# Performance work log

Measured on AMD Instinct MI355X. Metric: run time of the kernel, lower is better.

## Reference

```python
import jax, jax.numpy as jnp
import numpy as np

T = 8192        # tokens (batch*seq)
D = 1024        # d_model
H = 4096        # expert hidden = 4*d_model
E = 16          # num_expert
K = 2           # moe_top_k


def setup_inputs() -> dict:
    key = jax.random.key(0)
    ks = jax.random.split(key, 7)
    s_in = 1.0 / np.sqrt(D)
    s_h = 1.0 / np.sqrt(H)
    return {
        "moe_inp": jax.random.normal(ks[0], (T, D), dtype=jnp.float32),
        "Wg": jax.random.normal(ks[1], (D, E), dtype=jnp.float32) * s_in,
        "bg": jnp.zeros((E,), dtype=jnp.float32),
        "W1": jax.random.normal(ks[2], (E, D, H), dtype=jnp.float32) * s_in,
        "b1": jnp.zeros((E, H), dtype=jnp.float32),
        "W2": jax.random.normal(ks[3], (E, H, D), dtype=jnp.float32) * s_h,
        "b2": jnp.zeros((E, D), dtype=jnp.float32),
    }


def reference(moe_inp, Wg, bg, W1, b1, W2, b2):
    # --- NaiveGate: linear -> top-k -> softmax over selected logits ---
    logits = moe_inp @ Wg + bg                      # [T, E]
    topk_val, topk_idx = jax.lax.top_k(logits, K)   # [T, K]
    gate_score = jax.nn.softmax(topk_val, axis=-1)  # [T, K]

    # Per-(token, expert) combine weight: sum of gate scores of slots routed to e.
    # Equivalent to scatter(dispatch) -> expert MLP -> gather(combine) weighted sum.
    onehot = jax.nn.one_hot(topk_idx, E, dtype=moe_inp.dtype)  # [T, K, E]
    comb_w = jnp.einsum('tk,tke->te', gate_score, onehot)      # [T, E]

    out = jnp.zeros_like(moe_inp)
    for e in range(E):  # fixed small expert count
        h = jax.nn.relu(moe_inp @ W1[e] + b1[e])   # [T, H]
        y = h @ W2[e] + b2[e]                      # [T, D]
        out = out + comb_w[:, e:e + 1] * y
    return out
```

## Files before the change

kernel.cpp:

```cpp
#include <hip/hip_runtime.h>
#include <hip/hip_bf16.h>
#include <stdint.h>


#define Tn 8192
#define Dn 1024
#define Hn 4096
#define En 16

typedef __attribute__((ext_vector_type(8))) short bf16x8;
typedef __attribute__((ext_vector_type(4))) float f32x4;

__device__ __forceinline__ unsigned short f2bf(float f) {
    union { __hip_bfloat16 h; unsigned short u; } cv;
    cv.h = __float2bfloat16(f);
    return cv.u;
}
__device__ __forceinline__ float bf2f(unsigned short u) {
    union { unsigned int i; float f; } cv;
    cv.i = ((unsigned int)u) << 16;
    return cv.f;
}

__device__ __forceinline__ void gload_lds16(const void* gptr, void* lptr) {
    __builtin_amdgcn_global_load_lds(
        (const __attribute__((address_space(1))) uint32_t*)gptr,
        (__attribute__((address_space(3))) uint32_t*)lptr, 16, 0, 0);
}

__device__ __forceinline__ int find_e(const int* __restrict__ mb, int gm) {
    int e = 0;
#pragma unroll
    for (int i = 1; i < En; i++) e += (mb[i] <= gm) ? 1 : 0;
    return e;
}

__device__ __forceinline__ void waitvm0()  { asm volatile("s_waitcnt vmcnt(0)" ::: "memory"); }
__device__ __forceinline__ void barrier_raw() { asm volatile("s_barrier" ::: "memory"); }

__device__ __forceinline__ bool better(float va, int ia, float vb, int ib) {
    return (va > vb) || (va == vb && ia < ib);
}

__global__ __launch_bounds__(256) void gate_kernel(
    const float* __restrict__ x, const float* __restrict__ Wg,
    const float* __restrict__ bg,
    int* cnt, int* tok_e, int* tok_pos, float* tok_w)
{
    __shared__ float wgt[16 * 1028];
    int tid = threadIdx.x;
    int t0 = blockIdx.x * 16;

#pragma unroll
    for (int i = 0; i < 64; i++) {
        int idx = i * 256 + tid;
        int k = idx >> 4, e = idx & 15;
        wgt[e * 1028 + k] = Wg[idx];
    }
    __syncthreads();

    int tok = tid >> 4, e = tid & 15;
    const float4* xr = reinterpret_cast<const float4*>(x + (size_t)(t0 + tok) * Dn);
    const float4* wr = reinterpret_cast<const float4*>(&wgt[e * 1028]);
    float acc = 0.f;
#pragma unroll 8
    for (int q = 0; q < 256; q++) {
        float4 xv = xr[q], wv = wr[q];
        acc += xv.x * wv.x + xv.y * wv.y + xv.z * wv.z + xv.w * wv.w;
    }
    acc += bg[e];

    float v0 = acc, v1 = -1e30f;
    int i0 = e, i1 = -1;
#pragma unroll
    for (int m = 1; m < 16; m <<= 1) {
        float ov0 = __shfl_xor(v0, m, 16); int oi0 = __shfl_xor(i0, m, 16);
        float ov1 = __shfl_xor(v1, m, 16); int oi1 = __shfl_xor(i1, m, 16);
        if (better(ov0, oi0, v0, i0)) {
            if (better(v0, i0, ov1, oi1)) { v1 = v0; i1 = i0; }
            else                          { v1 = ov1; i1 = oi1; }
            v0 = ov0; i0 = oi0;
        } else if (better(ov0, oi0, v1, i1)) {
            v1 = ov0; i1 = oi0;
        }
    }
    if (e == 0) {
        float ex = __expf(v1 - v0);
        float w0 = 1.f / (1.f + ex);
        float w1 = ex / (1.f + ex);
        int p0 = atomicAdd(&cnt[i0], 1);
        int p1 = atomicAdd(&cnt[i1], 1);
        int t = t0 + tok;
        tok_e[t * 2 + 0] = i0; tok_e[t * 2 + 1] = i1;
        tok_pos[t * 2 + 0] = p0; tok_pos[t * 2 + 1] = p1;
        tok_w[t * 2 + 0] = w0; tok_w[t * 2 + 1] = w1;
    }
}

__global__ void scan_kernel(const int* cnt, int* base, int* mb)
{
    if (threadIdx.x == 0 && blockIdx.x == 0) {
        int b = 0, m = 0;
        for (int e = 0; e < En; e++) {
            base[e] = b; mb[e] = m;
            b += cnt[e];
            m += (cnt[e] + 255) >> 8;
        }
        base[En] = b; mb[En] = m;
    }
}

__global__ __launch_bounds__(256) void gather_kernel(
    const float* __restrict__ x, const int* tok_e, const int* tok_pos,
    const int* base, unsigned short* xg)
{
    int t = blockIdx.x; int tid = threadIdx.x;
    int e0 = tok_e[2 * t], e1 = tok_e[2 * t + 1];
    int r0 = base[e0] + tok_pos[2 * t];
    int r1 = base[e1] + tok_pos[2 * t + 1];
    float4 v = *reinterpret_cast<const float4*>(x + (size_t)t * Dn + tid * 4);
    ushort4 u;
    u.x = f2bf(v.x); u.y = f2bf(v.y); u.z = f2bf(v.z); u.w = f2bf(v.w);
    *reinterpret_cast<ushort4*>(xg + (size_t)r0 * Dn + tid * 4) = u;
    *reinterpret_cast<ushort4*>(xg + (size_t)r1 * Dn + tid * 4) = u;
}

__global__ __launch_bounds__(512) void convT_kernel(
    const float* __restrict__ src, unsigned short* __restrict__ dst, int R, int C)
{
    int e = blockIdx.z;
    const float* s = src + (size_t)e * R * C;
    unsigned short* d = dst + (size_t)e * R * C;
    __shared__ float tile[64][65];
    int r0 = blockIdx.y * 64, c0 = blockIdx.x * 64;
    int tr = threadIdx.x >> 4;
    int tc4 = (threadIdx.x & 15) * 4;
    float4 v0 = *reinterpret_cast<const float4*>(s + (size_t)(r0 + tr) * C + c0 + tc4);
    float4 v1 = *reinterpret_cast<const float4*>(s + (size_t)(r0 + tr + 32) * C + c0 + tc4);
    tile[tr][tc4 + 0] = v0.x; tile[tr][tc4 + 1] = v0.y;
    tile[tr][tc4 + 2] = v0.z; tile[tr][tc4 + 3] = v0.w;
    tile[tr + 32][tc4 + 0] = v1.x; tile[tr + 32][tc4 + 1] = v1.y;
    tile[tr + 32][tc4 + 2] = v1.z; tile[tr + 32][tc4 + 3] = v1.w;
    __syncthreads();
    ushort4 u0, u1;
    u0.x = f2bf(tile[tc4 + 0][tr]);      u1.x = f2bf(tile[tc4 + 0][tr + 32]);
    u0.y = f2bf(tile[tc4 + 1][tr]);      u1.y = f2bf(tile[tc4 + 1][tr + 32]);
    u0.z = f2bf(tile[tc4 + 2][tr]);      u1.z = f2bf(tile[tc4 + 2][tr + 32]);
    u0.w = f2bf(tile[tc4 + 3][tr]);      u1.w = f2bf(tile[tc4 + 3][tr + 32]);
    *reinterpret_cast<ushort4*>(d + (size_t)(c0 + tr) * R + r0 + tc4) = u0;
    *reinterpret_cast<ushort4*>(d + (size_t)(c0 + tr + 32) * R + r0 + tc4) = u1;
}

template<bool G1>
__global__ __launch_bounds__(512, 2) void gemmk_kernel(
    const unsigned short* __restrict__ Ag, const unsigned short* __restrict__ Bg,
    const float* __restrict__ bias, unsigned short* __restrict__ outb,
    size_t ystride,
    const int* __restrict__ cnt, const int* __restrict__ base,
    const int* __restrict__ mb)
{
    constexpr int KDIM = G1 ? Dn : Hn;
    constexpr int KLEN = G1 ? Dn : (Hn / 2);
    constexpr int NOUT = G1 ? Hn : Dn;
    constexpr int NT = KLEN / 64;
    __shared__ unsigned short ldsA[2][256 * 64];
    __shared__ unsigned short ldsB[2][256 * 64];

    int bid = blockIdx.x;
    int xcd = bid & 7;
    int slot = bid >> 3;
    int totalgm = mb[En];
    int rounds = G1 ? ((totalgm + 15) >> 4) : ((totalgm + 31) >> 5);

    int tid = threadIdx.x;
    int lane = tid & 63;
    int wid = tid >> 6;
    int wr = wid >> 2, wc = wid & 3;
    int lr16 = lane & 15, lk = lane >> 4;
    int lj = lk * 4;

    int r0t = tid >> 3;
    int col8 = (tid & 7) ^ (r0t & 7);

    int aoff[8][2], boff[4][2];
#pragma unroll
    for (int m = 0; m < 8; m++) {
        int row = wr * 128 + m * 16 + lr16;
#pragma unroll
        for (int kk = 0; kk < 2; kk++)
            aoff[m][kk] = row * 64 + (((kk * 4 + lk) ^ (row & 7)) << 3);
    }
#pragma unroll
    for (int n = 0; n < 4; n++) {
        int row = wc * 64 + n * 16 + lr16;
#pragma unroll
        for (int kk = 0; kk < 2; kk++)
            boff[n][kk] = row * 64 + (((kk * 4 + lk) ^ (row & 7)) << 3);
    }

    for (int r = 0; r < rounds; r++) {
        int gm, ntile, kh;
        if constexpr (G1) {
            gm = r * 16 + (slot >> 1);
            ntile = xcd * 2 + (slot & 1);
            kh = 0;
        } else {
            gm = r * 32 + slot;
            ntile = xcd >> 1;
            kh = xcd & 1;
        }
        if (gm >= totalgm) continue;

        int e = find_e(mb, gm);
        int mtile = gm - mb[e];
        int M_e = cnt[e];
        int m0 = mtile * 256, n0 = ntile * 256;
        int kbase = kh * KLEN;
        int rowbase0 = base[e] + m0;
        const unsigned short* Ab = Ag + (size_t)rowbase0 * KDIM + kbase;
        const unsigned short* Bb = Bg + (size_t)e * NOUT * KDIM + (size_t)n0 * KDIM + kbase;

        const unsigned short* aSrc = Ab + (size_t)r0t * KDIM + col8 * 8;
        const unsigned short* bSrc = Bb + (size_t)r0t * KDIM + col8 * 8;

        f32x4 acc[8][4];
#pragma unroll
        for (int m = 0; m < 8; m++)
#pragma unroll
            for (int n = 0; n < 4; n++) acc[m][n] = (f32x4){0.f, 0.f, 0.f, 0.f};

        auto stage = [&](int t) {
            char* sa = (char*)ldsA[t & 1];
            char* sb = (char*)ldsB[t & 1];
            int k0 = t * 64;
#pragma unroll
            for (int i = 0; i < 4; i++) {
                gload_lds16(aSrc + (size_t)(i * 64) * KDIM + k0, sa + (tid + i * 512) * 16);
                gload_lds16(bSrc + (size_t)(i * 64) * KDIM + k0, sb + (tid + i * 512) * 16);
            }
        };

        stage(0);

        for (int t = 0; t < NT; ++t) {
            waitvm0();
            barrier_raw();
            if (t + 1 < NT) stage(t + 1);
            asm volatile("" ::: "memory");
            const unsigned short* sa = ldsA[t & 1];
            const unsigned short* sb = ldsB[t & 1];
#pragma unroll
            for (int kk = 0; kk < 2; kk++) {
                bf16x8 a[4], b[4];
#pragma unroll
                for (int n = 0; n < 4; n++) b[n] = *(const bf16x8*)(sb + boff[n][kk]);
#pragma unroll
                for (int m = 0; m < 4; m++) a[m] = *(const bf16x8*)(sa + aoff[m][kk]);
                __builtin_amdgcn_s_setprio(1);
#pragma unroll
                for (int m = 0; m < 4; m++)
#pragma unroll
                    for (int n = 0; n < 4; n++)
                        acc[m][n] = __builtin_amdgcn_mfma_f32_16x16x32_bf16(b[n], a[m], acc[m][n], 0, 0, 0);
                __builtin_amdgcn_s_setprio(0);
#pragma unroll
                for (int m = 0; m < 4; m++) a[m] = *(const bf16x8*)(sa + aoff[m + 4][kk]);
                __builtin_amdgcn_s_setprio(1);
#pragma unroll
                for (int m = 0; m < 4; m++)
#pragma unroll
                    for (int n = 0; n < 4; n++)
                        acc[m + 4][n] = __builtin_amdgcn_mfma_f32_16x16x32_bf16(b[n], a[m], acc[m + 4][n], 0, 0, 0);
                __builtin_amdgcn_s_setprio(0);
            }
        }

        bool addb = G1 || (kh == 0);
        const float* be = bias + (size_t)e * NOUT;
        unsigned short* ob = outb + (G1 ? 0 : (size_t)kh * ystride);
#pragma unroll
        for (int m = 0; m < 8; m++) {
            int rt = wr * 128 + m * 16 + lr16;
            if (m0 + rt < M_e) {
                size_t rowoff = (size_t)(rowbase0 + rt) * NOUT;
#pragma unroll
                for (int n = 0; n < 4; n++) {
                    int col0 = n0 + wc * 64 + n * 16 + lj;
                    float4 bs = addb ? *reinterpret_cast<const float4*>(be + col0)
                                     : (float4){0.f, 0.f, 0.f, 0.f};
                    float v0 = acc[m][n][0] + bs.x;
                    float v1 = acc[m][n][1] + bs.y;
                    float v2 = acc[m][n][2] + bs.z;
                    float v3 = acc[m][n][3] + bs.w;
                    ushort4 u;
                    if constexpr (G1) {
                        u.x = f2bf(fmaxf(v0, 0.f));
                        u.y = f2bf(fmaxf(v1, 0.f));
                        u.z = f2bf(fmaxf(v2, 0.f));
                        u.w = f2bf(fmaxf(v3, 0.f));
                    } else {
                        u.x = f2bf(v0); u.y = f2bf(v1);
                        u.z = f2bf(v2); u.w = f2bf(v3);
                    }
                    *reinterpret_cast<ushort4*>(ob + rowoff + col0) = u;
                }
            }
        }
    }
}

__global__ __launch_bounds__(256) void combine_kernel(
    const unsigned short* __restrict__ y, size_t ystride,
    const int* __restrict__ tok_e, const int* __restrict__ tok_pos,
    const int* __restrict__ base, const float* __restrict__ tok_w,
    float* __restrict__ out)
{
    int t = blockIdx.x, tid = threadIdx.x;
    int e0 = tok_e[2 * t], e1 = tok_e[2 * t + 1];
    int r0 = base[e0] + tok_pos[2 * t];
    int r1 = base[e1] + tok_pos[2 * t + 1];
    float w0 = tok_w[2 * t], w1 = tok_w[2 * t + 1];
    const unsigned short* y1 = y + ystride;
    ushort4 a0 = *reinterpret_cast<const ushort4*>(y  + (size_t)r0 * Dn + tid * 4);
    ushort4 a1 = *reinterpret_cast<const ushort4*>(y1 + (size_t)r0 * Dn + tid * 4);
    ushort4 b0 = *reinterpret_cast<const ushort4*>(y  + (size_t)r1 * Dn + tid * 4);
    ushort4 b1 = *reinterpret_cast<const ushort4*>(y1 + (size_t)r1 * Dn + tid * 4);
    float4 o;
    o.x = w0 * (bf2f(a0.x) + bf2f(a1.x)) + w1 * (bf2f(b0.x) + bf2f(b1.x));
    o.y = w0 * (bf2f(a0.y) + bf2f(a1.y)) + w1 * (bf2f(b0.y) + bf2f(b1.y));
    o.z = w0 * (bf2f(a0.z) + bf2f(a1.z)) + w1 * (bf2f(b0.z) + bf2f(b1.z));
    o.w = w0 * (bf2f(a0.w) + bf2f(a1.w)) + w1 * (bf2f(b0.w) + bf2f(b1.w));
    *reinterpret_cast<float4*>(out + (size_t)t * Dn + tid * 4) = o;
}

extern "C" void kernel_launch(void* const* d_in, const int* in_sizes, int n_in,
                              void* d_out, int out_size, void* d_ws, size_t ws_size,
                              hipStream_t stream)
{
    const float* x  = (const float*)d_in[0];
    const float* Wg = (const float*)d_in[1];
    const float* bg = (const float*)d_in[2];
    const float* W1 = (const float*)d_in[3];
    const float* b1 = (const float*)d_in[4];
    const float* W2 = (const float*)d_in[5];
    const float* b2 = (const float*)d_in[6];
    float* out = (float*)d_out;

    char* ws = (char*)d_ws;
    size_t off = 0;
    auto alloc = [&](size_t bytes) {
        size_t o = off; off += (bytes + 255) & ~(size_t)255; return o;
    };
    const int ROWS = Tn * 2;
    const int RCAP = ROWS + 256;
    const size_t YSTR = (size_t)RCAP * Dn;

    unsigned short* Wt = (unsigned short*)(ws + alloc((size_t)En * Hn * Dn * 2));
    unsigned short* xg = (unsigned short*)(ws + alloc((size_t)RCAP * Dn * 2));
    unsigned short* hg = (unsigned short*)(ws + alloc((size_t)RCAP * Hn * 2));
    unsigned short* yv = (unsigned short*)(ws + alloc(2 * YSTR * 2));
    int*   cnt     = (int*)(ws + alloc(En * 4));
    int*   base    = (int*)(ws + alloc((En + 1) * 4));
    int*   mb      = (int*)(ws + alloc((En + 1) * 4));
    int*   tok_e   = (int*)(ws + alloc(Tn * 2 * 4));
    int*   tok_pos = (int*)(ws + alloc(Tn * 2 * 4));
    float* tok_w   = (float*)(ws + alloc(Tn * 2 * 4));
    (void)ws_size; (void)in_sizes; (void)n_in; (void)out_size;

    hipMemsetAsync(cnt, 0, En * 4, stream);

    gate_kernel<<<Tn / 16, 256, 0, stream>>>(x, Wg, bg, cnt, tok_e, tok_pos, tok_w);
    scan_kernel<<<1, 64, 0, stream>>>(cnt, base, mb);
    gather_kernel<<<Tn, 256, 0, stream>>>(x, tok_e, tok_pos, base, xg);

    convT_kernel<<<dim3(Hn / 64, Dn / 64, En), 512, 0, stream>>>(W1, Wt, Dn, Hn);
    gemmk_kernel<true><<<256, 512, 0, stream>>>(
        xg, Wt, b1, hg, 0, cnt, base, mb);

    convT_kernel<<<dim3(Dn / 64, Hn / 64, En), 512, 0, stream>>>(W2, Wt, Hn, Dn);
    gemmk_kernel<false><<<256, 512, 0, stream>>>(
        hg, Wt, b2, yv, YSTR, cnt, base, mb);

    combine_kernel<<<Tn, 256, 0, stream>>>(yv, YSTR, tok_e, tok_pos, base, tok_w, out);
}
```

Baseline: 753.1 us.

## Replace 256x256 grouped GEMM with persistent 128x128 triple-buffered kernel

Replaces the 256x256-tile, 512-thread grouped expert GEMM with a 128x128-tile, 256-thread persistent kernel. It uses a 3-stage LDS pipeline with BK=32, an XCD-aware tile swizzle, and a grid-stride loop over (m,n) tiles. It also drops the split-K in the second GEMM, so combine reads a single y buffer, and expert row padding shrinks to 128. The aim is less padding waste, better load balance and higher occupancy. The trade-off is lower per-tile data reuse and more tiles to schedule.

Result: no change. 742.7 us (-1.4%).

```diff
diff --git a/kernel.cpp b/kernel.cpp
--- a/kernel.cpp
+++ b/kernel.cpp
@@ -28,6 +28,13 @@
         (__attribute__((address_space(3))) uint32_t*)lptr, 16, 0, 0);
 }
 
+__device__ __forceinline__ int swz_tile(int v, int total) {
+    int q = total >> 3, r = total & 7;
+    int x = v & 7, k = v >> 3;
+    int b = (x < r) ? x * (q + 1) : r * (q + 1) + (x - r) * q;
+    return b + k;
+}
+
 __device__ __forceinline__ int find_e(const int* __restrict__ mb, int gm) {
     int e = 0;
 #pragma unroll
@@ -35,6 +42,7 @@
     return e;
 }
 
+__device__ __forceinline__ void waitvm4()  { asm volatile("s_waitcnt vmcnt(4)" ::: "memory"); }
 __device__ __forceinline__ void waitvm0()  { asm volatile("s_waitcnt vmcnt(0)" ::: "memory"); }
 __device__ __forceinline__ void barrier_raw() { asm volatile("s_barrier" ::: "memory"); }
 
@@ -104,7 +112,7 @@
         for (int e = 0; e < En; e++) {
             base[e] = b; mb[e] = m;
             b += cnt[e];
-            m += (cnt[e] + 255) >> 8;
+            m += (cnt[e] + 127) >> 7;
         }
         base[En] = b; mb[En] = m;
     }
@@ -152,142 +160,116 @@
 }
 
 template<bool G1>
-__global__ __launch_bounds__(512, 2) void gemmk_kernel(
+__global__ __launch_bounds__(256, 3) void gemm128_kernel(
     const unsigned short* __restrict__ Ag, const unsigned short* __restrict__ Bg,
     const float* __restrict__ bias, unsigned short* __restrict__ outb,
-    size_t ystride,
     const int* __restrict__ cnt, const int* __restrict__ base,
     const int* __restrict__ mb)
 {
     constexpr int KDIM = G1 ? Dn : Hn;
-    constexpr int KLEN = G1 ? Dn : (Hn / 2);
     constexpr int NOUT = G1 ? Hn : Dn;
-    constexpr int NT = KLEN / 64;
-    __shared__ unsigned short ldsA[2][256 * 64];
-    __shared__ unsigned short ldsB[2][256 * 64];
-
-    int bid = blockIdx.x;
-    int xcd = bid & 7;
-    int slot = bid >> 3;
+    constexpr int NTN = NOUT / 128;
+    constexpr int NT = KDIM / 32;
+    __shared__ unsigned short ldsA[3][128 * 32];
+    __shared__ unsigned short ldsB[3][128 * 32];
+
     int totalgm = mb[En];
-    int rounds = G1 ? ((totalgm + 15) >> 4) : ((totalgm + 31) >> 5);
+    int total = totalgm * NTN;
 
     int tid = threadIdx.x;
     int lane = tid & 63;
-    int wid = tid >> 6;
-    int wr = wid >> 2, wc = wid & 3;
+    int w = tid >> 6;
+    int wm = (w >> 1) * 64, wn = (w & 1) * 64;
     int lr16 = lane & 15, lk = lane >> 4;
     int lj = lk * 4;
 
-    int r0t = tid >> 3;
-    int col8 = (tid & 7) ^ (r0t & 7);
-
-    int aoff[8][2], boff[4][2];
-#pragma unroll
-    for (int m = 0; m < 8; m++) {
-        int row = wr * 128 + m * 16 + lr16;
-#pragma unroll
-        for (int kk = 0; kk < 2; kk++)
-            aoff[m][kk] = row * 64 + (((kk * 4 + lk) ^ (row & 7)) << 3);
+    int r0t = tid >> 2;
+    int r1t = (tid + 256) >> 2;
+    int col0 = (tid & 3) ^ (r0t & 3);
+    int col1 = (tid & 3) ^ (r1t & 3);
+
+    int aoff[4], boff[4];
+#pragma unroll
+    for (int m = 0; m < 4; m++) {
+        int row = wm + m * 16 + lr16;
+        aoff[m] = row * 32 + ((lk ^ (row & 3)) << 3);
     }
 #pragma unroll
     for (int n = 0; n < 4; n++) {
-        int row = wc * 64 + n * 16 + lr16;
-#pragma unroll
-        for (int kk = 0; kk < 2; kk++)
-            boff[n][kk] = row * 64 + (((kk * 4 + lk) ^ (row & 7)) << 3);
-    }
-
-    for (int r = 0; r < rounds; r++) {
-        int gm, ntile, kh;
-        if constexpr (G1) {
-            gm = r * 16 + (slot >> 1);
-            ntile = xcd * 2 + (slot & 1);
-            kh = 0;
-        } else {
-            gm = r * 32 + slot;
-            ntile = xcd >> 1;
-            kh = xcd & 1;
-        }
-        if (gm >= totalgm) continue;
-
+        int row = wn + n * 16 + lr16;
+        boff[n] = row * 32 + ((lk ^ (row & 3)) << 3);
+    }
+
+    for (int v = blockIdx.x; v < total; v += gridDim.x) {
+        int tile = swz_tile(v, total);
+        int nt = tile / totalgm;
+        int gm = tile - nt * totalgm;
         int e = find_e(mb, gm);
         int mtile = gm - mb[e];
         int M_e = cnt[e];
-        int m0 = mtile * 256, n0 = ntile * 256;
-        int kbase = kh * KLEN;
+        int m0 = mtile * 128, n0 = nt * 128;
         int rowbase0 = base[e] + m0;
-        const unsigned short* Ab = Ag + (size_t)rowbase0 * KDIM + kbase;
-        const unsigned short* Bb = Bg + (size_t)e * NOUT * KDIM + (size_t)n0 * KDIM + kbase;
-
-        const unsigned short* aSrc = Ab + (size_t)r0t * KDIM + col8 * 8;
-        const unsigned short* bSrc = Bb + (size_t)r0t * KDIM + col8 * 8;
-
-        f32x4 acc[8][4];
-#pragma unroll
-        for (int m = 0; m < 8; m++)
+        const unsigned short* Ab = Ag + (size_t)rowbase0 * KDIM;
+        const unsigned short* Bb = Bg + ((size_t)e * NOUT + n0) * KDIM;
+
+        const unsigned short* aS0 = Ab + (size_t)r0t * KDIM + col0 * 8;
+        const unsigned short* aS1 = Ab + (size_t)r1t * KDIM + col1 * 8;
+        const unsigned short* bS0 = Bb + (size_t)r0t * KDIM + col0 * 8;
+        const unsigned short* bS1 = Bb + (size_t)r1t * KDIM + col1 * 8;
+
+        f32x4 acc[4][4];
+#pragma unroll
+        for (int m = 0; m < 4; m++)
 #pragma unroll
             for (int n = 0; n < 4; n++) acc[m][n] = (f32x4){0.f, 0.f, 0.f, 0.f};
 
-        auto stage = [&](int t) {
-            char* sa = (char*)ldsA[t & 1];
-            char* sb = (char*)ldsB[t & 1];
-            int k0 = t * 64;
-#pragma unroll
-            for (int i = 0; i < 4; i++) {
-                gload_lds16(aSrc + (size_t)(i * 64) * KDIM + k0, sa + (tid + i * 512) * 16);
-                gload_lds16(bSrc + (size_t)(i * 64) * KDIM + k0, sb + (tid + i * 512) * 16);
-            }
+        auto stage = [&](int t, int sl) {
+            char* sa = (char*)ldsA[sl];
+            char* sb = (char*)ldsB[sl];
+            int k0 = t * 32;
+            gload_lds16(aS0 + k0, sa + tid * 16);
+            gload_lds16(aS1 + k0, sa + (tid + 256) * 16);
+            gload_lds16(bS0 + k0, sb + tid * 16);
+            gload_lds16(bS1 + k0, sb + (tid + 256) * 16);
         };
 
-        stage(0);
-
+        stage(0, 0);
+        stage(1, 1);
+
+        int cur = 0, nxt2 = 2;
         for (int t = 0; t < NT; ++t) {
-            waitvm0();
+            if (t + 1 < NT) waitvm4();
+            else            waitvm0();
             barrier_raw();
-            if (t + 1 < NT) stage(t + 1);
-            asm volatile("" ::: "memory");
-            const unsigned short* sa = ldsA[t & 1];
-            const unsigned short* sb = ldsB[t & 1];
-#pragma unroll
-            for (int kk = 0; kk < 2; kk++) {
-                bf16x8 a[4], b[4];
-#pragma unroll
-                for (int n = 0; n < 4; n++) b[n] = *(const bf16x8*)(sb + boff[n][kk]);
-#pragma unroll
-                for (int m = 0; m < 4; m++) a[m] = *(const bf16x8*)(sa + aoff[m][kk]);
-                __builtin_amdgcn_s_setprio(1);
-#pragma unroll
-                for (int m = 0; m < 4; m++)
-#pragma unroll
-                    for (int n = 0; n < 4; n++)
-                        acc[m][n] = __builtin_amdgcn_mfma_f32_16x16x32_bf16(b[n], a[m], acc[m][n], 0, 0, 0);
-                __builtin_amdgcn_s_setprio(0);
-#pragma unroll
-                for (int m = 0; m < 4; m++) a[m] = *(const bf16x8*)(sa + aoff[m + 4][kk]);
-                __builtin_amdgcn_s_setprio(1);
-#pragma unroll
-                for (int m = 0; m < 4; m++)
-#pragma unroll
-                    for (int n = 0; n < 4; n++)
-                        acc[m + 4][n] = __builtin_amdgcn_mfma_f32_16x16x32_bf16(b[n], a[m], acc[m + 4][n], 0, 0, 0);
-                __builtin_amdgcn_s_setprio(0);
-            }
+            if (t + 2 < NT) stage(t + 2, nxt2);
+            const unsigned short* sa = ldsA[cur];
+            const unsigned short* sb = ldsB[cur];
+            bf16x8 a[4], b[4];
+#pragma unroll
+            for (int n = 0; n < 4; n++) b[n] = *(const bf16x8*)(sb + boff[n]);
+#pragma unroll
+            for (int m = 0; m < 4; m++) a[m] = *(const bf16x8*)(sa + aoff[m]);
+            __builtin_amdgcn_s_setprio(1);
+#pragma unroll
+            for (int m = 0; m < 4; m++)
+#pragma unroll
+                for (int n = 0; n < 4; n++)
+                    acc[m][n] = __builtin_amdgcn_mfma_f32_16x16x32_bf16(b[n], a[m], acc[m][n], 0, 0, 0);
+            __builtin_amdgcn_s_setprio(0);
+            cur = (cur == 2) ? 0 : cur + 1;
+            nxt2 = (nxt2 == 2) ? 0 : nxt2 + 1;
         }
 
-        bool addb = G1 || (kh == 0);
         const float* be = bias + (size_t)e * NOUT;
-        unsigned short* ob = outb + (G1 ? 0 : (size_t)kh * ystride);
-#pragma unroll
-        for (int m = 0; m < 8; m++) {
-            int rt = wr * 128 + m * 16 + lr16;
+#pragma unroll
+        for (int m = 0; m < 4; m++) {
+            int rt = wm + m * 16 + lr16;
             if (m0 + rt < M_e) {
                 size_t rowoff = (size_t)(rowbase0 + rt) * NOUT;
 #pragma unroll
                 for (int n = 0; n < 4; n++) {
-                    int col0 = n0 + wc * 64 + n * 16 + lj;
-                    float4 bs = addb ? *reinterpret_cast<const float4*>(be + col0)
-                                     : (float4){0.f, 0.f, 0.f, 0.f};
+                    int col0e = n0 + wn + n * 16 + lj;
+                    float4 bs = *reinterpret_cast<const float4*>(be + col0e);
                     float v0 = acc[m][n][0] + bs.x;
                     float v1 = acc[m][n][1] + bs.y;
                     float v2 = acc[m][n][2] + bs.z;
@@ -302,7 +284,7 @@
                         u.x = f2bf(v0); u.y = f2bf(v1);
                         u.z = f2bf(v2); u.w = f2bf(v3);
                     }
-                    *reinterpret_cast<ushort4*>(ob + rowoff + col0) = u;
+                    *reinterpret_cast<ushort4*>(outb + rowoff + col0e) = u;
                 }
             }
         }
@@ -310,7 +292,7 @@
 }
 
 __global__ __launch_bounds__(256) void combine_kernel(
-    const unsigned short* __restrict__ y, size_t ystride,
+    const unsigned short* __restrict__ y,
     const int* __restrict__ tok_e, const int* __restrict__ tok_pos,
     const int* __restrict__ base, const float* __restrict__ tok_w,
     float* __restrict__ out)
@@ -320,16 +302,13 @@
     int r0 = base[e0] + tok_pos[2 * t];
     int r1 = base[e1] + tok_pos[2 * t + 1];
     float w0 = tok_w[2 * t], w1 = tok_w[2 * t + 1];
-    const unsigned short* y1 = y + ystride;
-    ushort4 a0 = *reinterpret_cast<const ushort4*>(y  + (size_t)r0 * Dn + tid * 4);
-    ushort4 a1 = *reinterpret_cast<const ushort4*>(y1 + (size_t)r0 * Dn + tid * 4);
-    ushort4 b0 = *reinterpret_cast<const ushort4*>(y  + (size_t)r1 * Dn + tid * 4);
-    ushort4 b1 = *reinterpret_cast<const ushort4*>(y1 + (size_t)r1 * Dn + tid * 4);
+    ushort4 a = *reinterpret_cast<const ushort4*>(y + (size_t)r0 * Dn + tid * 4);
+    ushort4 b = *reinterpret_cast<const ushort4*>(y + (size_t)r1 * Dn + tid * 4);
     float4 o;
-    o.x = w0 * (bf2f(a0.x) + bf2f(a1.x)) + w1 * (bf2f(b0.x) + bf2f(b1.x));
-    o.y = w0 * (bf2f(a0.y) + bf2f(a1.y)) + w1 * (bf2f(b0.y) + bf2f(b1.y));
-    o.z = w0 * (bf2f(a0.z) + bf2f(a1.z)) + w1 * (bf2f(b0.z) + bf2f(b1.z));
-    o.w = w0 * (bf2f(a0.w) + bf2f(a1.w)) + w1 * (bf2f(b0.w) + bf2f(b1.w));
+    o.x = w0 * bf2f(a.x) + w1 * bf2f(b.x);
+    o.y = w0 * bf2f(a.y) + w1 * bf2f(b.y);
+    o.z = w0 * bf2f(a.z) + w1 * bf2f(b.z);
+    o.w = w0 * bf2f(a.w) + w1 * bf2f(b.w);
     *reinterpret_cast<float4*>(out + (size_t)t * Dn + tid * 4) = o;
 }
 
@@ -353,12 +332,11 @@
     };
     const int ROWS = Tn * 2;
     const int RCAP = ROWS + 256;
-    const size_t YSTR = (size_t)RCAP * Dn;
 
     unsigned short* Wt = (unsigned short*)(ws + alloc((size_t)En * Hn * Dn * 2));
     unsigned short* xg = (unsigned short*)(ws + alloc((size_t)RCAP * Dn * 2));
     unsigned short* hg = (unsigned short*)(ws + alloc((size_t)RCAP * Hn * 2));
-    unsigned short* yv = (unsigned short*)(ws + alloc(2 * YSTR * 2));
+    unsigned short* yv = (unsigned short*)(ws + alloc((size_t)RCAP * Dn * 2));
     int*   cnt     = (int*)(ws + alloc(En * 4));
     int*   base    = (int*)(ws + alloc((En + 1) * 4));
     int*   mb      = (int*)(ws + alloc((En + 1) * 4));
@@ -374,12 +352,12 @@
     gather_kernel<<<Tn, 256, 0, stream>>>(x, tok_e, tok_pos, base, xg);
 
     convT_kernel<<<dim3(Hn / 64, Dn / 64, En), 512, 0, stream>>>(W1, Wt, Dn, Hn);
-    gemmk_kernel<true><<<256, 512, 0, stream>>>(
-        xg, Wt, b1, hg, 0, cnt, base, mb);
+    gemm128_kernel<true><<<768, 256, 0, stream>>>(
+        xg, Wt, b1, hg, cnt, base, mb);
 
     convT_kernel<<<dim3(Dn / 64, Hn / 64, En), 512, 0, stream>>>(W2, Wt, Hn, Dn);
-    gemmk_kernel<false><<<256, 512, 0, stream>>>(
-        hg, Wt, b2, yv, YSTR, cnt, base, mb);
-
-    combine_kernel<<<Tn, 256, 0, stream>>>(yv, YSTR, tok_e, tok_pos, base, tok_w, out);
-}
+    gemm128_kernel<false><<<768, 256, 0, stream>>>(
+        hg, Wt, b2, yv, cnt, base, mb);
+
+    combine_kernel<<<Tn, 256, 0, stream>>>(yv, tok_e, tok_pos, base, tok_w, out);
+}
```

## Use 1024-thread blocks with K=32 stages and swizzled persistent tile scheduling

Applied to the files above, without the earlier changes.

The expert GEMM kernel now runs 16 waves per block (1024 threads), each wave computing a 64x64 sub-tile of the 256x256 output, with K-steps of 32 instead of 64. LDS per stage drops to half, and each thread issues one async global-to-LDS load per operand per step. Tiles are handed out by a grid-stride loop over all (m-tile, n-tile/k-half) units, with an XCD-aware swizzle that gives each XCD a contiguous range of units for L2 locality. This trades fewer accumulators per wave and more waves for latency hiding against twice as many barriers per K and shorter MFMA bursts between syncs.

Result: slower. 777.8 us (+3.3%).

```diff
diff --git a/kernel.cpp b/kernel.cpp
--- a/kernel.cpp
+++ b/kernel.cpp
@@ -26,6 +26,13 @@
     __builtin_amdgcn_global_load_lds(
         (const __attribute__((address_space(1))) uint32_t*)gptr,
         (__attribute__((address_space(3))) uint32_t*)lptr, 16, 0, 0);
+}
+
+__device__ __forceinline__ int swz_tile(int v, int total) {
+    int q = total >> 3, r = total & 7;
+    int x = v & 7, k = v >> 3;
+    int b = (x < r) ? x * (q + 1) : r * (q + 1) + (x - r) * q;
+    return b + k;
 }
 
 __device__ __forceinline__ int find_e(const int* __restrict__ mb, int gm) {
@@ -152,7 +159,7 @@
 }
 
 template<bool G1>
-__global__ __launch_bounds__(512, 2) void gemmk_kernel(
+__global__ __launch_bounds__(1024, 2) void gemm256_kernel(
     const unsigned short* __restrict__ Ag, const unsigned short* __restrict__ Bg,
     const float* __restrict__ bias, unsigned short* __restrict__ outb,
     size_t ystride,
@@ -162,15 +169,13 @@
     constexpr int KDIM = G1 ? Dn : Hn;
     constexpr int KLEN = G1 ? Dn : (Hn / 2);
     constexpr int NOUT = G1 ? Hn : Dn;
-    constexpr int NT = KLEN / 64;
-    __shared__ unsigned short ldsA[2][256 * 64];
-    __shared__ unsigned short ldsB[2][256 * 64];
-
-    int bid = blockIdx.x;
-    int xcd = bid & 7;
-    int slot = bid >> 3;
+    constexpr int UPG  = G1 ? (Hn / 256) : (Dn / 256) * 2;
+    constexpr int NT = KLEN / 32;
+    __shared__ unsigned short ldsA[2][128 * 64];
+    __shared__ unsigned short ldsB[2][128 * 64];
+
     int totalgm = mb[En];
-    int rounds = G1 ? ((totalgm + 15) >> 4) : ((totalgm + 31) >> 5);
+    int total = totalgm * UPG;
 
     int tid = threadIdx.x;
     int lane = tid & 63;
@@ -179,65 +184,54 @@
     int lr16 = lane & 15, lk = lane >> 4;
     int lj = lk * 4;
 
-    int r0t = tid >> 3;
-    int col8 = (tid & 7) ^ (r0t & 7);
-
-    int aoff[8][2], boff[4][2];
-#pragma unroll
-    for (int m = 0; m < 8; m++) {
-        int row = wr * 128 + m * 16 + lr16;
-#pragma unroll
-        for (int kk = 0; kk < 2; kk++)
-            aoff[m][kk] = row * 64 + (((kk * 4 + lk) ^ (row & 7)) << 3);
+    int lrow = tid >> 3;
+    int chS = (tid & 7) ^ (lrow & 7);
+    int grow = lrow * 2 + (chS >> 2);
+    int kc = chS & 3;
+
+    int aoff[4], boff[4];
+#pragma unroll
+    for (int m = 0; m < 4; m++) {
+        int row = wr * 64 + m * 16 + lr16;
+        int lr = row >> 1;
+        aoff[m] = lr * 64 + (((((row & 1) << 2) | lk) ^ (lr & 7)) << 3);
     }
 #pragma unroll
     for (int n = 0; n < 4; n++) {
         int row = wc * 64 + n * 16 + lr16;
-#pragma unroll
-        for (int kk = 0; kk < 2; kk++)
-            boff[n][kk] = row * 64 + (((kk * 4 + lk) ^ (row & 7)) << 3);
-    }
-
-    for (int r = 0; r < rounds; r++) {
-        int gm, ntile, kh;
-        if constexpr (G1) {
-            gm = r * 16 + (slot >> 1);
-            ntile = xcd * 2 + (slot & 1);
-            kh = 0;
-        } else {
-            gm = r * 32 + slot;
-            ntile = xcd >> 1;
-            kh = xcd & 1;
-        }
-        if (gm >= totalgm) continue;
+        int lr = row >> 1;
+        boff[n] = lr * 64 + (((((row & 1) << 2) | lk) ^ (lr & 7)) << 3);
+    }
+
+    for (int v = blockIdx.x; v < total; v += gridDim.x) {
+        int u = swz_tile(v, total);
+        int pg = u / totalgm;
+        int gm = u - pg * totalgm;
+        int nt, kh;
+        if constexpr (G1) { nt = pg; kh = 0; }
+        else              { nt = pg >> 1; kh = pg & 1; }
 
         int e = find_e(mb, gm);
         int mtile = gm - mb[e];
         int M_e = cnt[e];
-        int m0 = mtile * 256, n0 = ntile * 256;
+        int m0 = mtile * 256, n0 = nt * 256;
         int kbase = kh * KLEN;
         int rowbase0 = base[e] + m0;
         const unsigned short* Ab = Ag + (size_t)rowbase0 * KDIM + kbase;
-        const unsigned short* Bb = Bg + (size_t)e * NOUT * KDIM + (size_t)n0 * KDIM + kbase;
-
-        const unsigned short* aSrc = Ab + (size_t)r0t * KDIM + col8 * 8;
-        const unsigned short* bSrc = Bb + (size_t)r0t * KDIM + col8 * 8;
-
-        f32x4 acc[8][4];
-#pragma unroll
-        for (int m = 0; m < 8; m++)
+        const unsigned short* Bb = Bg + ((size_t)e * NOUT + n0) * KDIM + kbase;
+        const unsigned short* aS = Ab + (size_t)grow * KDIM + kc * 8;
+        const unsigned short* bS = Bb + (size_t)grow * KDIM + kc * 8;
+
+        f32x4 acc[4][4];
+#pragma unroll
+        for (int m = 0; m < 4; m++)
 #pragma unroll
             for (int n = 0; n < 4; n++) acc[m][n] = (f32x4){0.f, 0.f, 0.f, 0.f};
 
         auto stage = [&](int t) {
-            char* sa = (char*)ldsA[t & 1];
-            char* sb = (char*)ldsB[t & 1];
-            int k0 = t * 64;
-#pragma unroll
-            for (int i = 0; i < 4; i++) {
-                gload_lds16(aSrc + (size_t)(i * 64) * KDIM + k0, sa + (tid + i * 512) * 16);
-                gload_lds16(bSrc + (size_t)(i * 64) * KDIM + k0, sb + (tid + i * 512) * 16);
-            }
+            int k0 = t * 32;
+            gload_lds16(aS + k0, (char*)ldsA[t & 1] + tid * 16);
+            gload_lds16(bS + k0, (char*)ldsB[t & 1] + tid * 16);
         };
 
         stage(0);
@@ -249,38 +243,26 @@
             asm volatile("" ::: "memory");
             const unsigned short* sa = ldsA[t & 1];
             const unsigned short* sb = ldsB[t & 1];
-#pragma unroll
-            for (int kk = 0; kk < 2; kk++) {
-                bf16x8 a[4], b[4];
-#pragma unroll
-                for (int n = 0; n < 4; n++) b[n] = *(const bf16x8*)(sb + boff[n][kk]);
-#pragma unroll
-                for (int m = 0; m < 4; m++) a[m] = *(const bf16x8*)(sa + aoff[m][kk]);
-                __builtin_amdgcn_s_setprio(1);
-#pragma unroll
-                for (int m = 0; m < 4; m++)
-#pragma unroll
-                    for (int n = 0; n < 4; n++)
-                        acc[m][n] = __builtin_amdgcn_mfma_f32_16x16x32_bf16(b[n], a[m], acc[m][n], 0, 0, 0);
-                __builtin_amdgcn_s_setprio(0);
-#pragma unroll
-                for (int m = 0; m < 4; m++) a[m] = *(const bf16x8*)(sa + aoff[m + 4][kk]);
-                __builtin_amdgcn_s_setprio(1);
-#pragma unroll
-                for (int m = 0; m < 4; m++)
-#pragma unroll
-                    for (int n = 0; n < 4; n++)
-                        acc[m + 4][n] = __builtin_amdgcn_mfma_f32_16x16x32_bf16(b[n], a[m], acc[m + 4][n], 0, 0, 0);
-                __builtin_amdgcn_s_setprio(0);
-            }
+            bf16x8 a[4], b[4];
+#pragma unroll
+            for (int n = 0; n < 4; n++) b[n] = *(const bf16x8*)(sb + boff[n]);
+#pragma unroll
+            for (int m = 0; m < 4; m++) a[m] = *(const bf16x8*)(sa + aoff[m]);
+            __builtin_amdgcn_s_setprio(1);
+#pragma unroll
+            for (int m = 0; m < 4; m++)
+#pragma unroll
+                for (int n = 0; n < 4; n++)
+                    acc[m][n] = __builtin_amdgcn_mfma_f32_16x16x32_bf16(b[n], a[m], acc[m][n], 0, 0, 0);
+            __builtin_amdgcn_s_setprio(0);
         }
 
         bool addb = G1 || (kh == 0);
         const float* be = bias + (size_t)e * NOUT;
         unsigned short* ob = outb + (G1 ? 0 : (size_t)kh * ystride);
 #pragma unroll
-        for (int m = 0; m < 8; m++) {
-            int rt = wr * 128 + m * 16 + lr16;
+        for (int m = 0; m < 4; m++) {
+            int rt = wr * 64 + m * 16 + lr16;
             if (m0 + rt < M_e) {
                 size_t rowoff = (size_t)(rowbase0 + rt) * NOUT;
 #pragma unroll
@@ -292,17 +274,17 @@
                     float v1 = acc[m][n][1] + bs.y;
                     float v2 = acc[m][n][2] + bs.z;
                     float v3 = acc[m][n][3] + bs.w;
-                    ushort4 u;
+                    ushort4 uo;
                     if constexpr (G1) {
-                        u.x = f2bf(fmaxf(v0, 0.f));
-                        u.y = f2bf(fmaxf(v1, 0.f));
-                        u.z = f2bf(fmaxf(v2, 0.f));
-                        u.w = f2bf(fmaxf(v3, 0.f));
+                        uo.x = f2bf(fmaxf(v0, 0.f));
+                        uo.y = f2bf(fmaxf(v1, 0.f));
+                        uo.z = f2bf(fmaxf(v2, 0.f));
+                        uo.w = f2bf(fmaxf(v3, 0.f));
                     } else {
-                        u.x = f2bf(v0); u.y = f2bf(v1);
-                        u.z = f2bf(v2); u.w = f2bf(v3);
+                        uo.x = f2bf(v0); uo.y = f2bf(v1);
+                        uo.z = f2bf(v2); uo.w = f2bf(v3);
                     }
-                    *reinterpret_cast<ushort4*>(ob + rowoff + col0) = u;
+                    *reinterpret_cast<ushort4*>(ob + rowoff + col0) = uo;
                 }
             }
         }
@@ -374,11 +356,11 @@
     gather_kernel<<<Tn, 256, 0, stream>>>(x, tok_e, tok_pos, base, xg);
 
     convT_kernel<<<dim3(Hn / 64, Dn / 64, En), 512, 0, stream>>>(W1, Wt, Dn, Hn);
-    gemmk_kernel<true><<<256, 512, 0, stream>>>(
+    gemm256_kernel<true><<<512, 1024, 0, stream>>>(
         xg, Wt, b1, hg, 0, cnt, base, mb);
 
     convT_kernel<<<dim3(Dn / 64, Hn / 64, En), 512, 0, stream>>>(W2, Wt, Hn, Dn);
-    gemmk_kernel<false><<<256, 512, 0, stream>>>(
+    gemm256_kernel<false><<<512, 1024, 0, stream>>>(
         hg, Wt, b2, yv, YSTR, cnt, base, mb);
 
     combine_kernel<<<Tn, 256, 0, stream>>>(yv, YSTR, tok_e, tok_pos, base, tok_w, out);
```
